# Optimization experiments

Hardware: AMD Instinct MI355X
Metric: run time of the kernel (lower is better)

The kernel has to match this reference:

```python
import jax, jax.numpy as jnp
import numpy as np

INV_SQRT2 = 0.7071067811865476  # 1/sqrt(2)


def haar_wavelet_transform(x):
    length = x.shape[-1]
    max_level = int(np.log2(length))  # static, from shape
    approximations = []
    for _ in range(max_level):
        even = x[..., 0::2]
        odd = x[..., 1::2]
        cA = (even - odd) * INV_SQRT2
        cD = (even + odd) * INV_SQRT2
        approximations.append(cA)
        x = cD
    approximations.append(x)
    return tuple(approximations)


def setup_inputs() -> dict:
    key = jax.random.key(0)
    x = jax.random.normal(key, (64, 64, 16384), dtype=jnp.float32)
    return {"x": x}


def reference(x):
    return haar_wavelet_transform(x)
```

## Files before the change

kernel.cpp:

```cpp
#include <hip/hip_runtime.h>


constexpr int ROW_LEN = 16384;
constexpr int LEVELS  = 14;
constexpr int NROWS   = 64 * 64;
constexpr int NT      = 256;

__global__ __launch_bounds__(NT) void haar_kernel(const float* __restrict__ in,
                                                  float* __restrict__ out) {
    __shared__ float lds[ROW_LEN / 8];

    const int row = blockIdx.x;
    const int tid = threadIdx.x;
    const float k = 0.70710678118654752440f;

    const float4* rin4 = (const float4*)(in + (size_t)row * ROW_LEN);
    float4* out1 = (float4*)(out + (size_t)row * (ROW_LEN / 2));
    float2* out2 = (float2*)(out + (size_t)NROWS * (ROW_LEN / 2)
                                 + (size_t)row * (ROW_LEN / 4));
    float*  out3 = out + (size_t)NROWS * (ROW_LEN / 2 + ROW_LEN / 4)
                       + (size_t)row * (ROW_LEN / 8);

    #pragma unroll
    for (int it = 0; it < ROW_LEN / (8 * NT); ++it) {
        int tp = it * NT + tid;
        float4 v0 = rin4[2 * tp];
        float4 v1 = rin4[2 * tp + 1];

        float4 ca1;
        ca1.x = (v0.x - v0.y) * k;
        ca1.y = (v0.z - v0.w) * k;
        ca1.z = (v1.x - v1.y) * k;
        ca1.w = (v1.z - v1.w) * k;
        float d0 = (v0.x + v0.y) * k;
        float d1 = (v0.z + v0.w) * k;
        float d2 = (v1.x + v1.y) * k;
        float d3 = (v1.z + v1.w) * k;

        float2 ca2;
        ca2.x = (d0 - d1) * k;
        ca2.y = (d2 - d3) * k;
        float e0 = (d0 + d1) * k;
        float e1 = (d2 + d3) * k;

        float ca3 = (e0 - e1) * k;
        float cd3 = (e0 + e1) * k;

        out1[tp] = ca1;
        out2[tp] = ca2;
        out3[tp] = ca3;
        lds[tp]  = cd3;
    }
    __syncthreads();

    size_t chunk_off = (size_t)NROWS * (ROW_LEN / 2 + ROW_LEN / 4 + ROW_LEN / 8);
    for (int L = 4; L <= LEVELS; ++L) {
        const int n_out  = ROW_LEN >> L;
        const int stride = 1 << (L - 4);
        float* outL = out + chunk_off + (size_t)row * n_out;
        for (int i = tid; i < n_out; i += NT) {
            const int base = i << (L - 3);
            const float even = lds[base];
            const float odd  = lds[base + stride];
            outL[i]   = (even - odd) * k;
            lds[base] = (even + odd) * k;
        }
        chunk_off += (size_t)NROWS * n_out;
        __syncthreads();
    }

    if (tid == 0) {
        out[chunk_off + row] = lds[0];
    }
}

extern "C" void kernel_launch(void* const* d_in, const int* in_sizes, int n_in,
                              void* d_out, int out_size, void* d_ws, size_t ws_size,
                              hipStream_t stream) {
    const float* x = (const float*)d_in[0];
    float* out = (float*)d_out;
    haar_kernel<<<dim3(NROWS), dim3(NT), 0, stream>>>(x, out);
}
```

Before: 432.1 us.

## Fuse four levels in registers, vectorize LDS levels, finish tail with wave shuffles

Each thread now loads 16 inputs and computes four Haar levels in registers before writing to LDS. It then runs three vectorized LDS levels with ping-pong buffers, and a single wavefront finishes the last six levels using __shfl with no further block barriers. Global loads and stores switch to nontemporal builtins. The aim is to cut the number of __syncthreads and strided scalar LDS passes from about eleven to three, trading for higher register use per thread.

```diff
diff --git a/kernel.cpp b/kernel.cpp
--- a/kernel.cpp
+++ b/kernel.cpp
@@ -1,76 +1,110 @@
 #include <hip/hip_runtime.h>
 
 
+typedef float f32x4 __attribute__((ext_vector_type(4)));
+typedef float f32x2 __attribute__((ext_vector_type(2)));
+
 constexpr int ROW_LEN = 16384;
-constexpr int LEVELS  = 14;
 constexpr int NROWS   = 64 * 64;
 constexpr int NT      = 256;
 
 __global__ __launch_bounds__(NT) void haar_kernel(const float* __restrict__ in,
                                                   float* __restrict__ out) {
-    __shared__ float lds[ROW_LEN / 8];
+    __shared__ __align__(16) float bufA[1024];
+    __shared__ __align__(16) float bufB[512];
 
     const int row = blockIdx.x;
     const int tid = threadIdx.x;
-    const float k = 0.70710678118654752440f;
+    const float K = 0.70710678118654752440f;
 
-    const float4* rin4 = (const float4*)(in + (size_t)row * ROW_LEN);
-    float4* out1 = (float4*)(out + (size_t)row * (ROW_LEN / 2));
-    float2* out2 = (float2*)(out + (size_t)NROWS * (ROW_LEN / 2)
-                                 + (size_t)row * (ROW_LEN / 4));
-    float*  out3 = out + (size_t)NROWS * (ROW_LEN / 2 + ROW_LEN / 4)
-                       + (size_t)row * (ROW_LEN / 8);
+    const f32x4* rin4 = (const f32x4*)(in + (size_t)row * ROW_LEN);
+
+    f32x4* o1 = (f32x4*)(out + (size_t)row * 8192);
+    f32x4* o2 = (f32x4*)(out + (size_t)NROWS * 8192  + (size_t)row * 4096);
+    f32x2* o3 = (f32x2*)(out + (size_t)NROWS * 12288 + (size_t)row * 2048);
+    float* o4 =          out + (size_t)NROWS * 14336 + (size_t)row * 1024;
 
     #pragma unroll
-    for (int it = 0; it < ROW_LEN / (8 * NT); ++it) {
-        int tp = it * NT + tid;
-        float4 v0 = rin4[2 * tp];
-        float4 v1 = rin4[2 * tp + 1];
+    for (int it = 0; it < ROW_LEN / (16 * NT); ++it) {
+        const int tp = it * NT + tid;
+        f32x4 v0 = __builtin_nontemporal_load(rin4 + 4 * tp + 0);
+        f32x4 v1 = __builtin_nontemporal_load(rin4 + 4 * tp + 1);
+        f32x4 v2 = __builtin_nontemporal_load(rin4 + 4 * tp + 2);
+        f32x4 v3 = __builtin_nontemporal_load(rin4 + 4 * tp + 3);
 
-        float4 ca1;
-        ca1.x = (v0.x - v0.y) * k;
-        ca1.y = (v0.z - v0.w) * k;
-        ca1.z = (v1.x - v1.y) * k;
-        ca1.w = (v1.z - v1.w) * k;
-        float d0 = (v0.x + v0.y) * k;
-        float d1 = (v0.z + v0.w) * k;
-        float d2 = (v1.x + v1.y) * k;
-        float d3 = (v1.z + v1.w) * k;
+        f32x4 ca1a = { (v0.x - v0.y) * K, (v0.z - v0.w) * K,
+                       (v1.x - v1.y) * K, (v1.z - v1.w) * K };
+        f32x4 ca1b = { (v2.x - v2.y) * K, (v2.z - v2.w) * K,
+                       (v3.x - v3.y) * K, (v3.z - v3.w) * K };
+        float d0 = (v0.x + v0.y) * K, d1 = (v0.z + v0.w) * K;
+        float d2 = (v1.x + v1.y) * K, d3 = (v1.z + v1.w) * K;
+        float d4 = (v2.x + v2.y) * K, d5 = (v2.z + v2.w) * K;
+        float d6 = (v3.x + v3.y) * K, d7 = (v3.z + v3.w) * K;
 
-        float2 ca2;
-        ca2.x = (d0 - d1) * k;
-        ca2.y = (d2 - d3) * k;
-        float e0 = (d0 + d1) * k;
-        float e1 = (d2 + d3) * k;
+        f32x4 ca2 = { (d0 - d1) * K, (d2 - d3) * K,
+                      (d4 - d5) * K, (d6 - d7) * K };
+        float e0 = (d0 + d1) * K, e1 = (d2 + d3) * K;
+        float e2 = (d4 + d5) * K, e3 = (d6 + d7) * K;
 
-        float ca3 = (e0 - e1) * k;
-        float cd3 = (e0 + e1) * k;
+        f32x2 ca3 = { (e0 - e1) * K, (e2 - e3) * K };
+        float f0 = (e0 + e1) * K, f1 = (e2 + e3) * K;
 
-        out1[tp] = ca1;
-        out2[tp] = ca2;
-        out3[tp] = ca3;
-        lds[tp]  = cd3;
+        float ca4 = (f0 - f1) * K;
+        float cd4 = (f0 + f1) * K;
+
+        __builtin_nontemporal_store(ca1a, o1 + 2 * tp);
+        __builtin_nontemporal_store(ca1b, o1 + 2 * tp + 1);
+        __builtin_nontemporal_store(ca2,  o2 + tp);
+        __builtin_nontemporal_store(ca3,  o3 + tp);
+        __builtin_nontemporal_store(ca4,  o4 + tp);
+        bufA[tp] = cd4;
     }
     __syncthreads();
 
-    size_t chunk_off = (size_t)NROWS * (ROW_LEN / 2 + ROW_LEN / 4 + ROW_LEN / 8);
-    for (int L = 4; L <= LEVELS; ++L) {
-        const int n_out  = ROW_LEN >> L;
-        const int stride = 1 << (L - 4);
-        float* outL = out + chunk_off + (size_t)row * n_out;
-        for (int i = tid; i < n_out; i += NT) {
-            const int base = i << (L - 3);
-            const float even = lds[base];
-            const float odd  = lds[base + stride];
-            outL[i]   = (even - odd) * k;
-            lds[base] = (even + odd) * k;
+    {
+        f32x4 v = ((const f32x4*)bufA)[tid];
+        f32x2 ca = { (v.x - v.y) * K, (v.z - v.w) * K };
+        f32x2 cd = { (v.x + v.y) * K, (v.z + v.w) * K };
+        f32x2* o5 = (f32x2*)(out + (size_t)NROWS * 15360 + (size_t)row * 512);
+        o5[tid] = ca;
+        ((f32x2*)bufB)[tid] = cd;
+    }
+    __syncthreads();
+
+    if (tid < 128) {
+        f32x4 v = ((const f32x4*)bufB)[tid];
+        f32x2 ca = { (v.x - v.y) * K, (v.z - v.w) * K };
+        f32x2 cd = { (v.x + v.y) * K, (v.z + v.w) * K };
+        f32x2* o6 = (f32x2*)(out + (size_t)NROWS * 15872 + (size_t)row * 256);
+        o6[tid] = ca;
+        ((f32x2*)bufA)[tid] = cd;
+    }
+    __syncthreads();
+
+    if (tid < 64) {
+        f32x4 v = ((const f32x4*)bufA)[tid];
+        f32x2 ca7 = { (v.x - v.y) * K, (v.z - v.w) * K };
+        f32x2* o7 = (f32x2*)(out + (size_t)NROWS * 16128 + (size_t)row * 128);
+        o7[tid] = ca7;
+        float cd7a = (v.x + v.y) * K;
+        float cd7b = (v.z + v.w) * K;
+
+        float* o8 = out + (size_t)NROWS * 16256 + (size_t)row * 64;
+        o8[tid] = (cd7a - cd7b) * K;
+        float x = (cd7a + cd7b) * K;
+
+        size_t chunk = (size_t)NROWS * 16320;
+        #pragma unroll
+        for (int L = 9; L <= 14; ++L) {
+            const int n = ROW_LEN >> L;
+            float even = __shfl(x, 2 * tid,     64);
+            float odd  = __shfl(x, 2 * tid + 1, 64);
+            float ca = (even - odd) * K;
+            x        = (even + odd) * K;
+            if (tid < n) out[chunk + (size_t)row * n + tid] = ca;
+            chunk += (size_t)NROWS * n;
         }
-        chunk_off += (size_t)NROWS * n_out;
-        __syncthreads();
-    }
-
-    if (tid == 0) {
-        out[chunk_off + row] = lds[0];
+        if (tid == 0) out[chunk + row] = x;
     }
 }
 
```

Result: slower. 450.8 us (+4.3%).
